# Optimization experiments

Hardware: AMD Instinct MI355X
Metric: run time of the kernel (lower is better)

## Reference

```python
import jax, jax.numpy as jnp
import numpy as np

# Model constants (hard-coded in the torch module / xLSTM config)
B, T, D, H, V = 512, 128, 128, 4, 30000
HD = D // H          # head dim = 32
K = 4                # causal conv1d kernel size
UP = 192             # gated FFN up dim: round_up(1.3*128, 64)
NB = 2               # num sLSTM blocks
EPS = 1e-5


def layernorm(x, w):
    mu = x.mean(-1, keepdims=True)
    var = x.var(-1, keepdims=True)
    return (x - mu) * jax.lax.rsqrt(var + EPS) * w


def setup_inputs() -> dict:
    key = jax.random.key(0)
    ks = iter(jax.random.split(key, 32))

    def rn(shape, s=0.05):
        return jax.random.normal(next(ks), shape, jnp.float32) * s

    tokens = jax.random.randint(next(ks), (B, T), 0, V)
    return {
        "tokens": tokens,
        "emb": rn((V, D), 0.02),
        "ln1_w": jnp.ones((NB, D)),
        "conv_w": rn((NB, D, K), 0.1),          # depthwise causal conv weights
        "conv_b": jnp.zeros((NB, D)),
        "Wi": rn((NB, H, HD, HD), 0.1),          # headwise gate projections
        "Wf": rn((NB, H, HD, HD), 0.1),
        "Wz": rn((NB, H, HD, HD), 0.1),
        "Wo": rn((NB, H, HD, HD), 0.1),
        "Rk": rn((NB, H, HD, 4 * HD), 0.1),      # per-head recurrent kernel
        "cell_b": jnp.zeros((NB, H, 4 * HD)),
        "gn_w": jnp.ones((NB, D)),               # multi-head (group) norm weight
        "ln2_w": jnp.ones((NB, D)),
        "ff_w1": rn((NB, D, 2 * UP), 0.05),      # gated FFN up proj
        "ff_b1": jnp.zeros((NB, 2 * UP)),
        "ff_w2": rn((NB, UP, D), 0.05),
        "ff_b2": jnp.zeros((NB, D)),
        "post_norm_w": jnp.ones((D,)),
        "cls_w1": rn((D, 64), 0.05),
        "cls_b1": jnp.zeros((64,)),
        "cls_w2": rn((64, 2), 0.05),
        "cls_b2": jnp.zeros((2,)),
    }


def slstm_layer(x, conv_w, conv_b, Wi, Wf, Wz, Wo, Rk, cell_b, gn_w):
    # x: [B,T,D]. Causal depthwise conv (left pad K-1) + swish.
    xp = jnp.pad(x, ((0, 0), (K - 1, 0), (0, 0)))
    conv = conv_b + sum(xp[:, k:k + T, :] * conv_w[:, k] for k in range(K))
    x_conv = jax.nn.silu(conv)
    xc = x_conv.reshape(B, T, H, HD)
    xh = x.reshape(B, T, H, HD)
    # i/f gates read the conv branch, z/o gates read x (xLSTM sLSTMLayer).
    i_in = jnp.einsum('bthd,hde->bthe', xc, Wi)
    f_in = jnp.einsum('bthd,hde->bthe', xc, Wf)
    z_in = jnp.einsum('bthd,hde->bthe', xh, Wz)
    o_in = jnp.einsum('bthd,hde->bthe', xh, Wo)
    gates = jnp.concatenate([i_in, f_in, z_in, o_in], -1)  # [B,T,H,4HD]
    gates = jnp.swapaxes(gates, 0, 1)                       # [T,B,H,4HD]

    def step(carry, g_t):
        h, c, n, m = carry  # each [B,H,HD]
        raw = g_t + jnp.einsum('bhd,hdg->bhg', h, Rk) + cell_b
        ir, fr, zr, og = jnp.split(raw, 4, axis=-1)
        # exponential gating with stabilizer state m
        m_new = jnp.maximum(fr + m, ir)
        ig = jnp.exp(ir - m_new)
        fg = jnp.exp(fr + m - m_new)
        c_new = fg * c + ig * jnp.tanh(zr)
        n_new = fg * n + ig
        h_new = jax.nn.sigmoid(og) * c_new / n_new
        return (h_new, c_new, n_new, m_new), h_new

    z0 = jnp.zeros((B, H, HD), x.dtype)
    _, ys = jax.lax.scan(step, (z0, z0, z0, z0), gates)
    y = jnp.swapaxes(ys, 0, 1)  # [B,T,H,HD]
    # multi-head layernorm (group norm over each head)
    mu = y.mean(-1, keepdims=True)
    var = y.var(-1, keepdims=True)
    yn = (y - mu) * jax.lax.rsqrt(var + EPS)
    return yn.reshape(B, T, D) * gn_w


def reference(tokens, emb, ln1_w, conv_w, conv_b, Wi, Wf, Wz, Wo, Rk, cell_b,
              gn_w, ln2_w, ff_w1, ff_b1, ff_w2, ff_b2, post_norm_w,
              cls_w1, cls_b1, cls_w2, cls_b2):
    x = emb[tokens]  # [B,T,D]
    for b in range(NB):
        x = x + slstm_layer(layernorm(x, ln1_w[b]), conv_w[b], conv_b[b],
                            Wi[b], Wf[b], Wz[b], Wo[b], Rk[b], cell_b[b], gn_w[b])
        h = layernorm(x, ln2_w[b]) @ ff_w1[b] + ff_b1[b]
        gate, up = jnp.split(h, 2, axis=-1)
        x = x + (jax.nn.gelu(gate) * up) @ ff_w2[b] + ff_b2[b]
    x = layernorm(x, post_norm_w)
    pooled = x.mean(axis=1)  # [B,D]
    h1 = jax.nn.relu(pooled @ cls_w1 + cls_b1)
    return h1 @ cls_w2 + cls_b2  # [B,2] logits
```

## Files before the change

### kernel.cpp

```cpp
#include <hip/hip_runtime.h>

typedef unsigned short u16;
typedef unsigned int u32;
typedef __attribute__((ext_vector_type(8))) short short8;
typedef __attribute__((ext_vector_type(4))) short s16x4;
typedef __attribute__((ext_vector_type(4))) float f32x4;
typedef __attribute__((ext_vector_type(2))) float f32x2;
typedef __attribute__((ext_vector_type(2))) int i32x2;

#define BB 512
#define TT 128
#define DD 128
#define HH 4
#define NBB 2
#define BT (BB*TT)
#define EPSF 1e-5f
#define LOG2E 1.4426950408889634f

__device__ __forceinline__ float bf2f(u16 u){ return __uint_as_float(((u32)u) << 16); }
__device__ __forceinline__ u16 f2bf(float f){
  u32 x = __float_as_uint(f);
  u32 r = x + 0x7fffu + ((x >> 16) & 1u);
  return (u16)(r >> 16);
}
__device__ __forceinline__ float bcastf(float v, int lane){
  return __uint_as_float(__builtin_amdgcn_readlane(__float_as_uint(v), lane));
}
__device__ __forceinline__ float gelu_fast(float x){
  float u = 0.7978845608028654f * (x + 0.044715f * x * x * x);
  float e2 = __builtin_amdgcn_exp2f(2.f * LOG2E * u);
  return x - x * __builtin_amdgcn_rcpf(e2 + 1.f);
}
#define DPP_ADD(v, ctrl, rmask, bc) \
  v += __int_as_float(__builtin_amdgcn_update_dpp(0, __float_as_int(v), (ctrl), (rmask), 0xf, (bc)))
__device__ __forceinline__ float wsum64(float v){
  DPP_ADD(v, 0x111, 0xf, true);
  DPP_ADD(v, 0x112, 0xf, true);
  DPP_ADD(v, 0x114, 0xf, true);
  DPP_ADD(v, 0x118, 0xf, true);
  DPP_ADD(v, 0x142, 0xa, false);
  DPP_ADD(v, 0x143, 0xc, false);
  return bcastf(v, 63);
}
__device__ __forceinline__ float rsum_rows01(float v){
  DPP_ADD(v, 0x111, 0xf, true);
  DPP_ADD(v, 0x112, 0xf, true);
  DPP_ADD(v, 0x114, 0xf, true);
  DPP_ADD(v, 0x118, 0xf, true);
  DPP_ADD(v, 0x142, 0xa, false);
  return v;
}
__device__ __forceinline__ float down32(float v){
  i32x2 r = __builtin_amdgcn_permlane32_swap(__float_as_int(v), __float_as_int(v), false, false);
  return __int_as_float(r.y);
}

__global__ __launch_bounds__(256) void k_convert(
    const float* __restrict__ ff_w1, const float* __restrict__ ff_w2,
    const float* __restrict__ Wi, const float* __restrict__ Wf,
    const float* __restrict__ Wz, const float* __restrict__ Wo,
    u16* __restrict__ w1T, u16* __restrict__ w2T,
    u16* __restrict__ gifT, u16* __restrict__ gzoT){
  int tid = blockIdx.x * 256 + threadIdx.x;
  const int n1 = NBB*384*128;
  if (tid < n1){
    int nb = tid / (384*128); int r = tid - nb*384*128; int n = r >> 7, k = r & 127;
    w1T[tid] = f2bf(ff_w1[(nb*128 + k)*384 + n]); return;
  }
  tid -= n1;
  const int n2 = NBB*128*192;
  if (tid < n2){
    int nb = tid / (128*192); int r = tid - nb*128*192; int n = r / 192, k = r - n*192;
    w2T[tid] = f2bf(ff_w2[(nb*192 + k)*128 + n]); return;
  }
  tid -= n2;
  const int n3 = NBB*HH*64*32;
  if (tid < n3){
    int nb = tid / (HH*64*32); int r = tid - nb*HH*64*32;
    int h = r >> 11; int r2 = r & 2047; int n = r2 >> 5, k = r2 & 31;
    const float* W = (n < 32) ? Wi : Wf; int nn = n & 31;
    gifT[tid] = f2bf(W[((nb*HH + h)*32 + k)*32 + nn]); return;
  }
  tid -= n3;
  if (tid < n3){
    int nb = tid / (HH*64*32); int r = tid - nb*HH*64*32;
    int h = r >> 11; int r2 = r & 2047; int n = r2 >> 5, k = r2 & 31;
    const float* W = (n < 32) ? Wz : Wo; int nn = n & 31;
    gzoT[tid] = f2bf(W[((nb*HH + h)*32 + k)*32 + nn]); return;
  }
}

__global__ __launch_bounds__(256) void k_lnconv(float* __restrict__ x,
    const int* __restrict__ tok, const float* __restrict__ emb,
    const float* __restrict__ ln1_w, const float* __restrict__ conv_w,
    const float* __restrict__ conv_b, u16* __restrict__ xn_bf,
    u16* __restrict__ xc_bf, int nb, int useemb){
  __shared__ float lnbuf[35][128];
  int b = blockIdx.x >> 2, tile = blockIdx.x & 3;
  int t0 = tile * 32;
  int wid = threadIdx.x >> 6, l = threadIdx.x & 63;
  for (int tt = wid; tt < 35; tt += 4){
    int t = t0 - 3 + tt;
    if (t < 0){
      lnbuf[tt][2*l] = 0.f; lnbuf[tt][2*l+1] = 0.f;
    } else {
      const float* src = useemb ? (emb + (size_t)tok[b*TT + t]*128)
                                : (x + (size_t)(b*TT + t)*128);
      float2 v = ((const float2*)src)[l];
      float s  = wsum64(v.x + v.y);
      float sq = wsum64(v.x*v.x + v.y*v.y);
      float mu = s * (1.f/128.f);
      float var = sq * (1.f/128.f) - mu*mu;
      float rs = rsqrtf(var + EPSF);
      float2 w = ((const float2*)(ln1_w + nb*128))[l];
      float y0 = (v.x - mu)*rs*w.x, y1 = (v.y - mu)*rs*w.y;
      lnbuf[tt][2*l] = y0; lnbuf[tt][2*l+1] = y1;
      if (tt >= 3){
        u32 pk = (u32)f2bf(y0) | ((u32)f2bf(y1) << 16);
        ((u32*)(xn_bf + (size_t)(b*TT + t)*128))[l] = pk;
        if (useemb) ((float2*)(x + (size_t)(b*TT + t)*128))[l] = v;
      }
    }
  }
  __syncthreads();
  for (int e = threadIdx.x; e < 32*128; e += 256){
    int tt = e >> 7, d = e & 127;
    float s = conv_b[nb*128 + d];
    #pragma unroll
    for (int k = 0; k < 4; k++)
      s += lnbuf[tt + k][d] * conv_w[(nb*128 + d)*4 + k];
    float sig = 1.f / (1.f + __expf(-s));
    xc_bf[(size_t)(b*TT + t0 + tt)*128 + d] = f2bf(s * sig);
  }
}

__global__ __launch_bounds__(256) void k_gates(const u16* __restrict__ xc_bf,
    const u16* __restrict__ xn_bf, const u16* __restrict__ gifT,
    const u16* __restrict__ gzoT, u16* __restrict__ gates, int nb){
  int m0 = blockIdx.x * 64;
  int b = m0 >> 7;
  int t00 = m0 & 127;
  int h = threadIdx.x >> 6, l = threadIdx.x & 63;
  short8 bfr[2][4];
  {
    const u16* B0 = gifT + (size_t)(nb*HH + h)*64*32;
    const u16* B1 = gzoT + (size_t)(nb*HH + h)*64*32;
    #pragma unroll
    for (int jt = 0; jt < 4; jt++){
      bfr[0][jt] = *(const short8*)(B0 + (jt*16 + (l & 15))*32 + (l >> 4)*8);
      bfr[1][jt] = *(const short8*)(B1 + (jt*16 + (l & 15))*32 + (l >> 4)*8);
    }
  }
  u16* gb = gates + (size_t)(b*HH + h)*TT*128;
  #pragma unroll
  for (int z = 0; z < 2; z++){
    const u16* A = z ? xn_bf : xc_bf;
    #pragma unroll
    for (int rg = 0; rg < 4; rg++){
      int r0 = m0 + rg*16;
      short8 a = *(const short8*)(A + (size_t)(r0 + (l & 15))*128 + h*32 + (l >> 4)*8);
      int tt = t00 + rg*16 + (l >> 4)*4;
      #pragma unroll
      for (int jt = 0; jt < 4; jt++){
        f32x4 acc = {0.f, 0.f, 0.f, 0.f};
        acc = __builtin_amdgcn_mfma_f32_16x16x32_bf16(a, bfr[z][jt], acc, 0, 0, 0);
        int cloc = z*64 + jt*16 + (l & 15);
        s16x4 pk;
        #pragma unroll
        for (int r = 0; r < 4; r++) pk[r] = (short)f2bf(acc[r]);
        *(s16x4*)(gb + ((size_t)(tt >> 3)*128 + cloc)*8 + (tt & 7)) = pk;
      }
    }
  }
}

__global__ __launch_bounds__(256, 2) void k_scan(const u16* __restrict__ gates,
    const float* __restrict__ Rk, const float* __restrict__ cell_b,
    const float* __restrict__ gn_w, float* __restrict__ x,
    float* __restrict__ dump, int nb){
  int wid = threadIdx.x >> 6, l = threadIdx.x & 63;
  int pair = blockIdx.x * 4 + wid;
  int b = pair >> 2, h = pair & 3;
  f32x2 rk[32];
  const float* Rkh = Rk + (size_t)(nb*HH + h)*32*128;
  #pragma unroll
  for (int d = 0; d < 32; d++){
    rk[d].x = Rkh[d*128 + l];
    rk[d].y = Rkh[d*128 + l + 64];
  }
  f32x2 cb = { cell_b[(nb*HH + h)*128 + l], cell_b[(nb*HH + h)*128 + l + 64] };
  int e = l & 31;
  bool lo = (l < 32);
  float gnw = gn_w[nb*128 + h*32 + e];
  float hs = 0.f, cs = 0.f, ns = 0.f, ms = 0.f;
  const u16* gbase = gates + (size_t)(b*HH + h)*TT*128;
  float* xp = lo ? (x + (size_t)(b*TT)*128 + h*32 + e) : (dump + pair*32 + e);
  int xstr = lo ? 128 : 0;
  float xq0 = xp[0];
  float xq1 = xp[xstr];
  float xq2 = xp[2*xstr];
  float xq3 = xp[3*xstr];
  short8 ga = *(const short8*)(gbase + (size_t)l*8);
  short8 gb = *(const short8*)(gbase + (size_t)(l + 64)*8);
  for (int t8 = 0; t8 < 16; t8++){
    short8 na  = *(const short8*)(gbase + ((size_t)(t8+1)*128 + l)*8);
    short8 nb2 = *(const short8*)(gbase + ((size_t)(t8+1)*128 + l + 64)*8);
    #pragma unroll
    for (int k = 0; k < 8; k++){
      float xcur = xq0;
      xq0 = xq1; xq1 = xq2; xq2 = xq3;
      xq3 = xp[4*xstr];
      f32x2 acc0 = { bf2f((u16)ga[k]) + cb.x, bf2f((u16)gb[k]) + cb.y };
      f32x2 acc1 = {0.f, 0.f}, acc2 = {0.f, 0.f}, acc3 = {0.f, 0.f};
      #pragma unroll
      for (int d = 0; d < 32; d += 4){
        float h0 = bcastf(hs, d),   h1 = bcastf(hs, d+1);
        float h2 = bcastf(hs, d+2), h3 = bcastf(hs, d+3);
        acc0 = __builtin_elementwise_fma((f32x2){h0,h0}, rk[d],   acc0);
        acc1 = __builtin_elementwise_fma((f32x2){h1,h1}, rk[d+1], acc1);
        acc2 = __builtin_elementwise_fma((f32x2){h2,h2}, rk[d+2], acc2);
        acc3 = __builtin_elementwise_fma((f32x2){h3,h3}, rk[d+3], acc3);
      }
      f32x2 rr = (acc0 + acc1) + (acc2 + acc3);
      float r0 = rr.x, r1 = rr.y;
      float fx = down32(r0);
      float ox = down32(r1);
      float mnew = fmaxf(fx + ms, r0);
      float ig = __builtin_amdgcn_exp2f((r0 - mnew) * LOG2E);
      float fg = __builtin_amdgcn_exp2f((fx + ms - mnew) * LOG2E);
      float e2 = __builtin_amdgcn_exp2f(2.f * LOG2E * r1);
      float th = fmaf(-2.f, __builtin_amdgcn_rcpf(e2 + 1.f), 1.f);
      cs = fmaf(fg, cs, ig * th);
      ns = fmaf(fg, ns, ig);
      ms = mnew;
      float se = __builtin_amdgcn_exp2f(-ox * LOG2E);
      hs = cs * __builtin_amdgcn_rcpf(fmaf(ns, se, ns));
      float s = rsum_rows01(hs);
      float sq = rsum_rows01(hs * hs);
      float mu = bcastf(s, 31) * (1.f/32.f);
      float var = bcastf(sq, 31) * (1.f/32.f) - mu*mu;
      float yn = (hs - mu) * __builtin_amdgcn_rsqf(var + EPSF) * gnw;
      xp[0] = xcur + yn;
      xp += xstr;
    }
    ga = na; gb = nb2;
  }
}

__global__ __launch_bounds__(512, 4) void k_ffn(float* __restrict__ x,
    const float* __restrict__ ln2_w, const u16* __restrict__ w1T,
    const float* __restrict__ ff_b1, const u16* __restrict__ w2T,
    const float* __restrict__ ff_b2, int nb){
  __shared__ u16 xln[64][136];
  __shared__ u16 hbuf[64][392];
  int m0 = blockIdx.x * 64;
  int w = threadIdx.x >> 6, l = threadIdx.x & 63;
  short8 w1f[3][4];
  const u16* W1 = w1T + (size_t)nb*384*128;
  #pragma unroll
  for (int j = 0; j < 3; j++)
    #pragma unroll
    for (int c = 0; c < 4; c++)
      w1f[j][c] = *(const short8*)(W1 + (size_t)((3*w + j)*16 + (l & 15))*128 + c*32 + (l >> 4)*8);
  short8 w2f[6];
  const u16* W2 = w2T + (size_t)nb*128*192;
  #pragma unroll
  for (int c = 0; c < 6; c++)
    w2f[c] = *(const short8*)(W2 + (size_t)(w*16 + (l & 15))*192 + c*32 + (l >> 4)*8);
  float2 lw = ((const float2*)(ln2_w + nb*128))[l];
  #pragma unroll
  for (int rr = 0; rr < 8; rr++){
    int row = w*8 + rr;
    float2 v = ((const float2*)(x + (size_t)(m0 + row)*128))[l];
    float s  = wsum64(v.x + v.y);
    float sq = wsum64(v.x*v.x + v.y*v.y);
    float mu = s * (1.f/128.f);
    float var = sq * (1.f/128.f) - mu*mu;
    float rs = rsqrtf(var + EPSF);
    ((u32*)xln[row])[l] = (u32)f2bf((v.x - mu)*rs*lw.x)
                        | ((u32)f2bf((v.y - mu)*rs*lw.y) << 16);
  }
  __syncthreads();
  #pragma unroll
  for (int rg = 0; rg < 4; rg++){
    short8 a[4];
    #pragma unroll
    for (int c = 0; c < 4; c++)
      a[c] = *(const short8*)(&xln[rg*16 + (l & 15)][c*32 + (l >> 4)*8]);
    #pragma unroll
    for (int j = 0; j < 3; j++){
      f32x4 acc = {0.f, 0.f, 0.f, 0.f};
      #pragma unroll
      for (int c = 0; c < 4; c++)
        acc = __builtin_amdgcn_mfma_f32_16x16x32_bf16(a[c], w1f[j][c], acc, 0, 0, 0);
      int col = (3*w + j)*16 + (l & 15);
      float bb = ff_b1[nb*384 + col];
      #pragma unroll
      for (int r = 0; r < 4; r++){
        int row = rg*16 + (l >> 4)*4 + r;
        hbuf[row][col] = f2bf(acc[r] + bb);
      }
    }
  }
  __syncthreads();
  {
    int row = threadIdx.x >> 3;
    int k0 = (threadIdx.x & 7) * 24;
    #pragma unroll
    for (int j2 = 0; j2 < 24; j2++){
      int k = k0 + j2;
      float gt = bf2f(hbuf[row][k]);
      float u = bf2f(hbuf[row][k + 192]);
      hbuf[row][k] = f2bf(gelu_fast(gt) * u);
    }
  }
  __syncthreads();
  #pragma unroll
  for (int rg = 0; rg < 4; rg++){
    f32x4 acc = {0.f, 0.f, 0.f, 0.f};
    #pragma unroll
    for (int c = 0; c < 6; c++){
      short8 a = *(const short8*)(&hbuf[rg*16 + (l & 15)][c*32 + (l >> 4)*8]);
      acc = __builtin_amdgcn_mfma_f32_16x16x32_bf16(a, w2f[c], acc, 0, 0, 0);
    }
    int col = w*16 + (l & 15);
    float bb = ff_b2[nb*128 + col];
    #pragma unroll
    for (int r = 0; r < 4; r++){
      int row = m0 + rg*16 + (l >> 4)*4 + r;
      x[(size_t)row*128 + col] += acc[r] + bb;
    }
  }
}

__global__ __launch_bounds__(256) void k_pool_cls(const float* __restrict__ x,
    const float* __restrict__ pw, const float* __restrict__ w1,
    const float* __restrict__ b1, const float* __restrict__ w2,
    const float* __restrict__ b2, float* __restrict__ out){
  __shared__ float red[4][128];
  __shared__ float pooled[128];
  __shared__ float h1s[64];
  int b = blockIdx.x;
  int wid = threadIdx.x >> 6, l = threadIdx.x & 63;
  float2 w = ((const float2*)pw)[l];
  float ax = 0.f, ay = 0.f;
  for (int t = wid; t < TT; t += 4){
    float2 v = ((const float2*)(x + (size_t)(b*TT + t)*128))[l];
    float s  = wsum64(v.x + v.y);
    float sq = wsum64(v.x*v.x + v.y*v.y);
    float mu = s * (1.f/128.f);
    float var = sq * (1.f/128.f) - mu*mu;
    float rs = rsqrtf(var + EPSF);
    ax += (v.x - mu)*rs*w.x;
    ay += (v.y - mu)*rs*w.y;
  }
  red[wid][2*l] = ax; red[wid][2*l+1] = ay;
  __syncthreads();
  if (threadIdx.x < 128){
    int d = threadIdx.x;
    pooled[d] = (red[0][d] + red[1][d] + red[2][d] + red[3][d]) * (1.f/128.f);
  }
  __syncthreads();
  if (threadIdx.x < 64){
    int j = threadIdx.x;
    float s = b1[j];
    for (int d = 0; d < 128; d++) s += pooled[d] * w1[d*64 + j];
    h1s[j] = fmaxf(s, 0.f);
  }
  __syncthreads();
  if (threadIdx.x < 2){
    int j = threadIdx.x;
    float s = b2[j];
    for (int k = 0; k < 64; k++) s += h1s[k] * w2[k*2 + j];
    out[b*2 + j] = s;
  }
}

extern "C" void kernel_launch(void* const* d_in, const int* in_sizes, int n_in,
                              void* d_out, int out_size, void* d_ws, size_t ws_size,
                              hipStream_t stream){
  const int*   tok    = (const int*)d_in[0];
  const float* emb    = (const float*)d_in[1];
  const float* ln1_w  = (const float*)d_in[2];
  const float* conv_w = (const float*)d_in[3];
  const float* conv_b = (const float*)d_in[4];
  const float* Wi     = (const float*)d_in[5];
  const float* Wf     = (const float*)d_in[6];
  const float* Wz     = (const float*)d_in[7];
  const float* Wo     = (const float*)d_in[8];
  const float* Rk     = (const float*)d_in[9];
  const float* cell_b = (const float*)d_in[10];
  const float* gn_w   = (const float*)d_in[11];
  const float* ln2_w  = (const float*)d_in[12];
  const float* ff_w1  = (const float*)d_in[13];
  const float* ff_b1  = (const float*)d_in[14];
  const float* ff_w2  = (const float*)d_in[15];
  const float* ff_b2  = (const float*)d_in[16];
  const float* postw  = (const float*)d_in[17];
  const float* cw1    = (const float*)d_in[18];
  const float* cb1    = (const float*)d_in[19];
  const float* cw2    = (const float*)d_in[20];
  const float* cb2    = (const float*)d_in[21];
  float* out = (float*)d_out;

  char* ws = (char*)d_ws;
  size_t off = 0;
  float* x      = (float*)(ws + off); off += (size_t)BT*128*4;
  u16*   xn_bf  = (u16*)(ws + off);   off += (size_t)BT*128*2;
  u16*   xc_bf  = (u16*)(ws + off);   off += (size_t)BT*128*2;
  u16*   gates  = (u16*)(ws + off);   off += (size_t)BT*512*2;
  u16*   w1T    = (u16*)(ws + off);   off += (size_t)NBB*384*128*2;
  u16*   w2T    = (u16*)(ws + off);   off += (size_t)NBB*128*192*2;
  u16*   gifT   = (u16*)(ws + off);   off += (size_t)NBB*HH*64*32*2;
  u16*   gzoT   = (u16*)(ws + off);   off += (size_t)NBB*HH*64*32*2;
  float* dump   = (float*)xn_bf;

  k_convert<<<704, 256, 0, stream>>>(ff_w1, ff_w2, Wi, Wf, Wz, Wo, w1T, w2T, gifT, gzoT);
  for (int nb = 0; nb < NBB; nb++){
    k_lnconv<<<BB*4, 256, 0, stream>>>(x, tok, emb, ln1_w, conv_w, conv_b,
                                       xn_bf, xc_bf, nb, nb == 0 ? 1 : 0);
    k_gates<<<BT/64, 256, 0, stream>>>(xc_bf, xn_bf, gifT, gzoT, gates, nb);
    k_scan<<<512, 256, 0, stream>>>(gates, Rk, cell_b, gn_w, x, dump, nb);
    k_ffn<<<BT/64, 512, 0, stream>>>(x, ln2_w, w1T, ff_b1, w2T, ff_b2, nb);
  }
  k_pool_cls<<<BB, 256, 0, stream>>>(x, postw, cw1, cb1, cw2, cb2, out);
}
```

Baseline: 297.7 us.

## Fuse gate projection MFMA into the sLSTM scan kernel via LDS staging

Computes the headwise i/f/z/o gate projections with MFMA inside the scan kernel, one 32-timestep chunk at a time, and stages them in a per-wave LDS tile. The separate gates kernel and its large bf16 gates buffer in global memory are removed. This avoids writing and re-reading the gates through HBM and drops one launch per block. The cost is extra registers and LDS in the latency-bound scan kernel, plus serial MFMA work between recurrence chunks. The dump scratch moves to its own buffer because xn_bf is now read by the scan.

New measurement: 273.3 us. 1.09x faster.

```diff
diff --git a/kernel.cpp b/kernel.cpp
--- a/kernel.cpp
+++ b/kernel.cpp
@@ -134,13 +134,23 @@
   }
 }
 
-__global__ __launch_bounds__(256) void k_gates(const u16* __restrict__ xc_bf,
+__global__ __launch_bounds__(256, 2) void k_scan(const u16* __restrict__ xc_bf,
     const u16* __restrict__ xn_bf, const u16* __restrict__ gifT,
-    const u16* __restrict__ gzoT, u16* __restrict__ gates, int nb){
-  int m0 = blockIdx.x * 64;
-  int b = m0 >> 7;
-  int t00 = m0 & 127;
-  int h = threadIdx.x >> 6, l = threadIdx.x & 63;
+    const u16* __restrict__ gzoT, const float* __restrict__ Rk,
+    const float* __restrict__ cell_b, const float* __restrict__ gn_w,
+    float* __restrict__ x, float* __restrict__ dump, int nb){
+  __shared__ u16 glds[4][128][36];
+  int wid = threadIdx.x >> 6, l = threadIdx.x & 63;
+  int pair = blockIdx.x * 4 + wid;
+  int b = pair >> 2, h = pair & 3;
+  u16 (*gw)[36] = glds[wid];
+  f32x2 rk[32];
+  const float* Rkh = Rk + (size_t)(nb*HH + h)*32*128;
+  #pragma unroll
+  for (int d = 0; d < 32; d++){
+    rk[d].x = Rkh[d*128 + l];
+    rk[d].y = Rkh[d*128 + l + 64];
+  }
   short8 bfr[2][4];
   {
     const u16* B0 = gifT + (size_t)(nb*HH + h)*64*32;
@@ -150,100 +160,98 @@
       bfr[0][jt] = *(const short8*)(B0 + (jt*16 + (l & 15))*32 + (l >> 4)*8);
       bfr[1][jt] = *(const short8*)(B1 + (jt*16 + (l & 15))*32 + (l >> 4)*8);
     }
-  }
-  u16* gb = gates + (size_t)(b*HH + h)*TT*128;
-  #pragma unroll
-  for (int z = 0; z < 2; z++){
-    const u16* A = z ? xn_bf : xc_bf;
-    #pragma unroll
-    for (int rg = 0; rg < 4; rg++){
-      int r0 = m0 + rg*16;
-      short8 a = *(const short8*)(A + (size_t)(r0 + (l & 15))*128 + h*32 + (l >> 4)*8);
-      int tt = t00 + rg*16 + (l >> 4)*4;
-      #pragma unroll
-      for (int jt = 0; jt < 4; jt++){
-        f32x4 acc = {0.f, 0.f, 0.f, 0.f};
-        acc = __builtin_amdgcn_mfma_f32_16x16x32_bf16(a, bfr[z][jt], acc, 0, 0, 0);
-        int cloc = z*64 + jt*16 + (l & 15);
-        s16x4 pk;
-        #pragma unroll
-        for (int r = 0; r < 4; r++) pk[r] = (short)f2bf(acc[r]);
-        *(s16x4*)(gb + ((size_t)(tt >> 3)*128 + cloc)*8 + (tt & 7)) = pk;
-      }
-    }
-  }
-}
-
-__global__ __launch_bounds__(256, 2) void k_scan(const u16* __restrict__ gates,
-    const float* __restrict__ Rk, const float* __restrict__ cell_b,
-    const float* __restrict__ gn_w, float* __restrict__ x,
-    float* __restrict__ dump, int nb){
-  int wid = threadIdx.x >> 6, l = threadIdx.x & 63;
-  int pair = blockIdx.x * 4 + wid;
-  int b = pair >> 2, h = pair & 3;
-  f32x2 rk[32];
-  const float* Rkh = Rk + (size_t)(nb*HH + h)*32*128;
-  #pragma unroll
-  for (int d = 0; d < 32; d++){
-    rk[d].x = Rkh[d*128 + l];
-    rk[d].y = Rkh[d*128 + l + 64];
   }
   f32x2 cb = { cell_b[(nb*HH + h)*128 + l], cell_b[(nb*HH + h)*128 + l + 64] };
   int e = l & 31;
   bool lo = (l < 32);
   float gnw = gn_w[nb*128 + h*32 + e];
   float hs = 0.f, cs = 0.f, ns = 0.f, ms = 0.f;
-  const u16* gbase = gates + (size_t)(b*HH + h)*TT*128;
+  const u16* baseA0 = xc_bf + ((size_t)(b*TT) + (l & 15))*128 + h*32 + (l >> 4)*8;
+  const u16* baseA1 = xn_bf + ((size_t)(b*TT) + (l & 15))*128 + h*32 + (l >> 4)*8;
+  short8 afr[2][2];
+  #pragma unroll
+  for (int rg = 0; rg < 2; rg++){
+    afr[0][rg] = *(const short8*)(baseA0 + (size_t)(rg*16)*128);
+    afr[1][rg] = *(const short8*)(baseA1 + (size_t)(rg*16)*128);
+  }
   float* xp = lo ? (x + (size_t)(b*TT)*128 + h*32 + e) : (dump + pair*32 + e);
   int xstr = lo ? 128 : 0;
   float xq0 = xp[0];
   float xq1 = xp[xstr];
   float xq2 = xp[2*xstr];
   float xq3 = xp[3*xstr];
-  short8 ga = *(const short8*)(gbase + (size_t)l*8);
-  short8 gb = *(const short8*)(gbase + (size_t)(l + 64)*8);
-  for (int t8 = 0; t8 < 16; t8++){
-    short8 na  = *(const short8*)(gbase + ((size_t)(t8+1)*128 + l)*8);
-    short8 nb2 = *(const short8*)(gbase + ((size_t)(t8+1)*128 + l + 64)*8);
-    #pragma unroll
-    for (int k = 0; k < 8; k++){
-      float xcur = xq0;
-      xq0 = xq1; xq1 = xq2; xq2 = xq3;
-      xq3 = xp[4*xstr];
-      f32x2 acc0 = { bf2f((u16)ga[k]) + cb.x, bf2f((u16)gb[k]) + cb.y };
-      f32x2 acc1 = {0.f, 0.f}, acc2 = {0.f, 0.f}, acc3 = {0.f, 0.f};
+  for (int ct = 0; ct < 4; ct++){
+    #pragma unroll
+    for (int z = 0; z < 2; z++){
       #pragma unroll
-      for (int d = 0; d < 32; d += 4){
-        float h0 = bcastf(hs, d),   h1 = bcastf(hs, d+1);
-        float h2 = bcastf(hs, d+2), h3 = bcastf(hs, d+3);
-        acc0 = __builtin_elementwise_fma((f32x2){h0,h0}, rk[d],   acc0);
-        acc1 = __builtin_elementwise_fma((f32x2){h1,h1}, rk[d+1], acc1);
-        acc2 = __builtin_elementwise_fma((f32x2){h2,h2}, rk[d+2], acc2);
-        acc3 = __builtin_elementwise_fma((f32x2){h3,h3}, rk[d+3], acc3);
+      for (int rg = 0; rg < 2; rg++){
+        short8 a = afr[z][rg];
+        int tloc = rg*16 + (l >> 4)*4;
+        #pragma unroll
+        for (int jt = 0; jt < 4; jt++){
+          f32x4 acc = {0.f, 0.f, 0.f, 0.f};
+          acc = __builtin_amdgcn_mfma_f32_16x16x32_bf16(a, bfr[z][jt], acc, 0, 0, 0);
+          int cloc = z*64 + jt*16 + (l & 15);
+          s16x4 pk;
+          #pragma unroll
+          for (int r = 0; r < 4; r++) pk[r] = (short)f2bf(acc[r]);
+          *(s16x4*)(&gw[cloc][tloc]) = pk;
+        }
       }
-      f32x2 rr = (acc0 + acc1) + (acc2 + acc3);
-      float r0 = rr.x, r1 = rr.y;
-      float fx = down32(r0);
-      float ox = down32(r1);
-      float mnew = fmaxf(fx + ms, r0);
-      float ig = __builtin_amdgcn_exp2f((r0 - mnew) * LOG2E);
-      float fg = __builtin_amdgcn_exp2f((fx + ms - mnew) * LOG2E);
-      float e2 = __builtin_amdgcn_exp2f(2.f * LOG2E * r1);
-      float th = fmaf(-2.f, __builtin_amdgcn_rcpf(e2 + 1.f), 1.f);
-      cs = fmaf(fg, cs, ig * th);
-      ns = fmaf(fg, ns, ig);
-      ms = mnew;
-      float se = __builtin_amdgcn_exp2f(-ox * LOG2E);
-      hs = cs * __builtin_amdgcn_rcpf(fmaf(ns, se, ns));
-      float s = rsum_rows01(hs);
-      float sq = rsum_rows01(hs * hs);
-      float mu = bcastf(s, 31) * (1.f/32.f);
-      float var = bcastf(sq, 31) * (1.f/32.f) - mu*mu;
-      float yn = (hs - mu) * __builtin_amdgcn_rsqf(var + EPSF) * gnw;
-      xp[0] = xcur + yn;
-      xp += xstr;
-    }
-    ga = na; gb = nb2;
+    }
+    if (ct < 3){
+      #pragma unroll
+      for (int rg = 0; rg < 2; rg++){
+        afr[0][rg] = *(const short8*)(baseA0 + (size_t)((ct+1)*32 + rg*16)*128);
+        afr[1][rg] = *(const short8*)(baseA1 + (size_t)((ct+1)*32 + rg*16)*128);
+      }
+    }
+    for (int t8g = 0; t8g < 4; t8g++){
+      s16x4 galo = *(const s16x4*)(&gw[l][t8g*8]);
+      s16x4 gahi = *(const s16x4*)(&gw[l][t8g*8 + 4]);
+      s16x4 gblo = *(const s16x4*)(&gw[l + 64][t8g*8]);
+      s16x4 gbhi = *(const s16x4*)(&gw[l + 64][t8g*8 + 4]);
+      #pragma unroll
+      for (int k = 0; k < 8; k++){
+        u16 g0 = (u16)(k < 4 ? galo[k & 3] : gahi[k & 3]);
+        u16 g1 = (u16)(k < 4 ? gblo[k & 3] : gbhi[k & 3]);
+        float xcur = xq0;
+        xq0 = xq1; xq1 = xq2; xq2 = xq3;
+        xq3 = xp[4*xstr];
+        f32x2 acc0 = { bf2f(g0) + cb.x, bf2f(g1) + cb.y };
+        f32x2 acc1 = {0.f, 0.f}, acc2 = {0.f, 0.f}, acc3 = {0.f, 0.f};
+        #pragma unroll
+        for (int d = 0; d < 32; d += 4){
+          float h0 = bcastf(hs, d),   h1 = bcastf(hs, d+1);
+          float h2 = bcastf(hs, d+2), h3 = bcastf(hs, d+3);
+          acc0 = __builtin_elementwise_fma((f32x2){h0,h0}, rk[d],   acc0);
+          acc1 = __builtin_elementwise_fma((f32x2){h1,h1}, rk[d+1], acc1);
+          acc2 = __builtin_elementwise_fma((f32x2){h2,h2}, rk[d+2], acc2);
+          acc3 = __builtin_elementwise_fma((f32x2){h3,h3}, rk[d+3], acc3);
+        }
+        f32x2 rr = (acc0 + acc1) + (acc2 + acc3);
+        float r0 = rr.x, r1 = rr.y;
+        float fx = down32(r0);
+        float ox = down32(r1);
+        float mnew = fmaxf(fx + ms, r0);
+        float ig = __builtin_amdgcn_exp2f((r0 - mnew) * LOG2E);
+        float fg = __builtin_amdgcn_exp2f((fx + ms - mnew) * LOG2E);
+        float e2 = __builtin_amdgcn_exp2f(2.f * LOG2E * r1);
+        float th = fmaf(-2.f, __builtin_amdgcn_rcpf(e2 + 1.f), 1.f);
+        cs = fmaf(fg, cs, ig * th);
+        ns = fmaf(fg, ns, ig);
+        ms = mnew;
+        float se = __builtin_amdgcn_exp2f(-ox * LOG2E);
+        hs = cs * __builtin_amdgcn_rcpf(fmaf(ns, se, ns));
+        float s = rsum_rows01(hs);
+        float sq = rsum_rows01(hs * hs);
+        float mu = bcastf(s, 31) * (1.f/32.f);
+        float var = bcastf(sq, 31) * (1.f/32.f) - mu*mu;
+        float yn = (hs - mu) * __builtin_amdgcn_rsqf(var + EPSF) * gnw;
+        xp[0] = xcur + yn;
+        xp += xstr;
+      }
+    }
   }
 }
 
@@ -406,21 +414,20 @@
   char* ws = (char*)d_ws;
   size_t off = 0;
   float* x      = (float*)(ws + off); off += (size_t)BT*128*4;
+  float* dump   = (float*)(ws + off); off += (size_t)2048*32*4;
   u16*   xn_bf  = (u16*)(ws + off);   off += (size_t)BT*128*2;
   u16*   xc_bf  = (u16*)(ws + off);   off += (size_t)BT*128*2;
-  u16*   gates  = (u16*)(ws + off);   off += (size_t)BT*512*2;
   u16*   w1T    = (u16*)(ws + off);   off += (size_t)NBB*384*128*2;
   u16*   w2T    = (u16*)(ws + off);   off += (size_t)NBB*128*192*2;
   u16*   gifT   = (u16*)(ws + off);   off += (size_t)NBB*HH*64*32*2;
   u16*   gzoT   = (u16*)(ws + off);   off += (size_t)NBB*HH*64*32*2;
-  float* dump   = (float*)xn_bf;
 
   k_convert<<<704, 256, 0, stream>>>(ff_w1, ff_w2, Wi, Wf, Wz, Wo, w1T, w2T, gifT, gzoT);
   for (int nb = 0; nb < NBB; nb++){
     k_lnconv<<<BB*4, 256, 0, stream>>>(x, tok, emb, ln1_w, conv_w, conv_b,
                                        xn_bf, xc_bf, nb, nb == 0 ? 1 : 0);
-    k_gates<<<BT/64, 256, 0, stream>>>(xc_bf, xn_bf, gifT, gzoT, gates, nb);
-    k_scan<<<512, 256, 0, stream>>>(gates, Rk, cell_b, gn_w, x, dump, nb);
+    k_scan<<<512, 256, 0, stream>>>(xc_bf, xn_bf, gifT, gzoT, Rk, cell_b,
+                                    gn_w, x, dump, nb);
     k_ffn<<<BT/64, 512, 0, stream>>>(x, ln2_w, w1T, ff_b1, w2T, ff_b2, nb);
   }
   k_pool_cls<<<BB, 256, 0, stream>>>(x, postw, cw1, cb1, cw2, cb2, out);
```
